# Kernel tuning notes

Hardware: AMD Instinct MI355X
Metric: run time of the kernel (lower is better)

## Reference

```python
import jax, jax.numpy as jnp
import numpy as np

S, P, T, E, H = 32, 48, 8, 64, 64      # scenes, peds/scene, obs_len, embedding_dim, h_dim
D1, D2 = 512, 1024                      # mlp_pre_pool hidden / bottleneck dims
B = S * P
TOTAL_LEN = 20                          # obs_len + pred_len (8 + 12)


def setup_inputs() -> dict:
    key = jax.random.key(0)
    ks = jax.random.split(key, 10)
    h_states = jax.random.normal(ks[0], (1, B, H), jnp.float32)
    end_pos = jax.random.normal(ks[1], (B, 2), jnp.float32)
    traj = jax.random.normal(ks[2], (TOTAL_LEN, B, 2), jnp.float32)
    traj_weight = jax.random.uniform(ks[3], (S, P * P, 2, T), jnp.float32)
    starts = jnp.arange(S, dtype=jnp.int32) * P
    seq_start_end = jnp.stack([starts, starts + P], axis=1)  # uniform scenes of P peds
    # learned params
    W_se = jax.random.normal(ks[4], (T * E, 2 * T), jnp.float32) * 0.05  # spatial_embedding
    b_se = jnp.zeros((T * E,), jnp.float32)
    W1 = jax.random.normal(ks[5], (D1, T * E + H), jnp.float32) * 0.05   # 576 -> 512
    b1 = jnp.zeros((D1,), jnp.float32)
    W2 = jax.random.normal(ks[6], (D2, D1), jnp.float32) * 0.05          # 512 -> 1024
    b2 = jnp.zeros((D2,), jnp.float32)
    return {"h_states": h_states, "seq_start_end": seq_start_end, "end_pos": end_pos,
            "traj": traj, "traj_weight": traj_weight, "mlp_pre_pool_dim_0": T * E,
            "W_se": W_se, "b_se": b_se, "W1": W1, "b1": b1, "W2": W2, "b2": b2}


def reference(h_states, seq_start_end, end_pos, traj, traj_weight, mlp_pre_pool_dim_0,
              W_se, b_se, W1, b1, W2, b2):
    # obs_traj: (obs_len, B, 2) -> (B, T, 2) -> per-scene (S, P, T, 2)
    obs = traj[:T].transpose(1, 0, 2).reshape(S, P, T, 2)
    h = h_states.reshape(S, P, H)
    # pairwise history differences: row (i, j) = obs[j] - obs[i]  (gather-diff)
    rel = obs[:, None, :, :, :] - obs[:, :, None, :, :]          # (S, i, j, T, 2)
    rel = rel.reshape(S, P, P, 2 * T)                            # flatten (T,2) -> 2T
    emb = rel @ W_se.T + b_se                                    # (S, P, P, T*E)
    # traj_weight[i]: (P*P, 2, T) -> permute(0,2,1) -> tile channel to E -> flatten
    w = jnp.transpose(traj_weight, (0, 1, 3, 2))                 # (S, P*P, T, 2)
    w = jnp.tile(w, (1, 1, 1, E // 2)).reshape(S, P, P, T * E)
    emb = w * emb
    # curr_hidden_1: hidden of ped j broadcast over i
    hj = jnp.broadcast_to(h[:, None, :, :], (S, P, P, H))
    x = jnp.concatenate([emb, hj], axis=-1)                      # (S, P, P, 576)
    x = jax.nn.relu(x @ W1.T + b1)                               # (S, P, P, 512)
    x = jax.nn.relu(x @ W2.T + b2)                               # (S, P, P, 1024)
    pool_h = x.max(axis=2)                                       # max over j
    return pool_h.reshape(S * P, D2)
```

## Files before the change

kernel.cpp:

```cpp
#include <hip/hip_runtime.h>
#include <hip/hip_bf16.h>
#include <stdint.h>

#define S_  32
#define P_  48
#define T_  8
#define E_  64
#define H_  64
#define D1_ 512
#define D2_ 1024
#define B_  (S_*P_)
#define M_  (S_*P_*P_)
#define K1_ 576
#define KE_ 512

typedef __attribute__((ext_vector_type(8))) short  short8;
typedef __attribute__((ext_vector_type(8))) __bf16 bf16x8;
typedef __attribute__((ext_vector_type(4))) float  f32x4;
typedef __attribute__((ext_vector_type(8))) float  f32x8;

__device__ inline short f2bf(float x) {
  union { float f; unsigned u; } v; v.f = x;
  unsigned r = v.u + 0x7FFFu + ((v.u >> 16) & 1u);
  return (short)(r >> 16);
}

__device__ inline void async16(const void* g, void* l) {
  __builtin_amdgcn_global_load_lds(
      (const __attribute__((address_space(1))) void*)g,
      (__attribute__((address_space(3))) void*)l, 16, 0, 0);
}

__device__ inline f32x4 mfma16(short8 a, short8 b, f32x4 c) {
  return __builtin_amdgcn_mfma_f32_16x16x32_bf16(
      __builtin_bit_cast(bf16x8, a), __builtin_bit_cast(bf16x8, b), c, 0, 0, 0);
}

__global__ __launch_bounds__(256) void k_cvt_w(const float* __restrict__ W1,
                                               const float* __restrict__ W2,
                                               short* __restrict__ W1b,
                                               short* __restrict__ W2b) {
  int idx = blockIdx.x * 256 + threadIdx.x;
  if (idx < D1_ * K1_) W1b[idx] = f2bf(W1[idx]);
  int idx2 = idx - D1_ * K1_;
  if (idx2 >= 0 && idx2 < D2_ * D1_) W2b[idx2] = f2bf(W2[idx2]);
}

__global__ __launch_bounds__(256) void k_oW(const float* __restrict__ traj,
                                            const float* __restrict__ Wse,
                                            float* __restrict__ oW) {
  int bid = blockIdx.x;
  int p = bid >> 1;
  int n = ((bid & 1) << 8) + threadIdx.x;
  float obs[16];
#pragma unroll
  for (int t = 0; t < T_; ++t) {
    obs[2*t]   = traj[(t*B_ + p)*2 + 0];
    obs[2*t+1] = traj[(t*B_ + p)*2 + 1];
  }
  float acc = 0.f;
#pragma unroll
  for (int k = 0; k < 16; ++k) acc += obs[k] * Wse[n*16 + k];
  oW[p*KE_ + n] = acc;
}

__global__ __launch_bounds__(256) void k_build_x(const float* __restrict__ tw,
                                                 const float* __restrict__ h,
                                                 const float* __restrict__ bse,
                                                 const float* __restrict__ oW,
                                                 short* __restrict__ X) {
  int tid = threadIdx.x;
  int wid = tid >> 6, lane = tid & 63;
  int row = blockIdx.x * 4 + wid;
  int s   = row / (P_ * P_);
  int rem = row - s * (P_ * P_);
  int i   = rem / P_;
  int j   = rem - i * P_;
  int bi = s * P_ + i, bj = s * P_ + j;

  const float* twq = tw + (size_t)(s * (P_*P_) + rem) * 16;
  int t = lane >> 3;
  float w0 = twq[t];
  float w1 = twq[8 + t];

  int n0 = lane * 8;
  f32x8 vj = *(const f32x8*)&oW[(size_t)bj * KE_ + n0];
  f32x8 vi = *(const f32x8*)&oW[(size_t)bi * KE_ + n0];
  f32x8 vb = *(const f32x8*)&bse[n0];
  short8 o;
#pragma unroll
  for (int k = 0; k < 8; ++k) {
    float e = (vj[k] - vi[k] + vb[k]) * ((k & 1) ? w1 : w0);
    o[k] = f2bf(e);
  }
  *(short8*)&X[(size_t)row * K1_ + n0] = o;

  if (lane < 8) {
    f32x8 vh = *(const f32x8*)&h[(size_t)bj * H_ + lane * 8];
    short8 oh;
#pragma unroll
    for (int k = 0; k < 8; ++k) oh[k] = f2bf(vh[k]);
    *(short8*)&X[(size_t)row * K1_ + KE_ + lane * 8] = oh;
  }
}

__global__ __launch_bounds__(512, 2) void k_gemm1(const short* __restrict__ X,
                                                  const short* __restrict__ W1b,
                                                  const float* __restrict__ b1,
                                                  short* __restrict__ X1) {
  __shared__ short Abuf[2][256 * 64];
  __shared__ short Bbuf[2][256 * 64];
  int tid = threadIdx.x;
  int wid = tid >> 6, lane = tid & 63;
  int wgid = (blockIdx.x & 7) * 72 + (blockIdx.x >> 3);
  int tm = wgid >> 1, tn = wgid & 1;
  int brow = tm * 256, bcol = tn * 256;
  int wr = wid >> 2, wc = wid & 3;
  int lr = lane & 15, lhi = lane >> 4;
  int sx = lr & 7;

  f32x4 acc[8][4];
#pragma unroll
  for (int m = 0; m < 8; ++m)
#pragma unroll
    for (int n = 0; n < 4; ++n) acc[m][n] = (f32x4){0.f, 0.f, 0.f, 0.f};

  auto stage = [&](int buf, int k0) {
#pragma unroll
    for (int it = 0; it < 4; ++it) {
      int fg = it * 512 + tid;
      int r = fg >> 3, gs = (fg & 7) ^ (r & 7);
      async16(&X  [(size_t)(brow + r) * K1_ + k0 + (gs << 3)], &Abuf[buf][fg * 8]);
    }
#pragma unroll
    for (int it = 0; it < 4; ++it) {
      int fg = it * 512 + tid;
      int r = fg >> 3, gs = (fg & 7) ^ (r & 7);
      async16(&W1b[(size_t)(bcol + r) * K1_ + k0 + (gs << 3)], &Bbuf[buf][fg * 8]);
    }
  };
  auto compute = [&](int buf) {
#pragma unroll
    for (int kk = 0; kk < 2; ++kk) {
      int gr = kk * 4 + lhi;
      short8 a[8], b[4];
#pragma unroll
      for (int m = 0; m < 8; ++m)
        a[m] = *(const short8*)&Abuf[buf][(wr*128 + m*16 + lr) * 64 + ((gr ^ sx) << 3)];
#pragma unroll
      for (int n = 0; n < 4; ++n)
        b[n] = *(const short8*)&Bbuf[buf][(wc*64 + n*16 + lr) * 64 + ((gr ^ sx) << 3)];
      __builtin_amdgcn_s_setprio(1);
#pragma unroll
      for (int m = 0; m < 8; ++m)
#pragma unroll
        for (int n = 0; n < 4; ++n)
          acc[m][n] = mfma16(a[m], b[n], acc[m][n]);
      __builtin_amdgcn_s_setprio(0);
    }
  };

  stage(0, 0);
  asm volatile("s_waitcnt vmcnt(0)" ::: "memory");
  __builtin_amdgcn_s_barrier();
  for (int t = 0; t < 9; ++t) {
    int cur = t & 1;
    if (t + 1 < 9) stage(cur ^ 1, (t + 1) * 64);
    compute(cur);
    asm volatile("s_waitcnt vmcnt(0)" ::: "memory");
    __builtin_amdgcn_s_barrier();
  }

#pragma unroll
  for (int n = 0; n < 4; ++n) {
    int gcol = bcol + wc*64 + n*16 + lr;
    float bias = b1[gcol];
#pragma unroll
    for (int m = 0; m < 8; ++m) {
      int grow0 = brow + wr*128 + m*16 + lhi*4;
#pragma unroll
      for (int q = 0; q < 4; ++q) {
        float v = acc[m][n][q] + bias;
        v = v > 0.f ? v : 0.f;
        X1[(size_t)(grow0 + q) * D1_ + gcol] = f2bf(v);
      }
    }
  }
}

__global__ __launch_bounds__(512, 2) void k_gemm2(const short* __restrict__ X1,
                                                  const short* __restrict__ W2b,
                                                  const float* __restrict__ b2,
                                                  float* __restrict__ out) {
  __shared__ short Abuf[2][192 * 64];
  __shared__ short Bbuf[2][256 * 64];
  int tid = threadIdx.x;
  int wid = tid >> 6, lane = tid & 63;
  int wgid = (blockIdx.x & 7) * 192 + (blockIdx.x >> 3);
  int tm = wgid >> 2, tn = wgid & 3;
  int brow = tm * 192, bcol = tn * 256;
  int wr = wid >> 2, wc = wid & 3;
  int lr = lane & 15, lhi = lane >> 4;
  int sx = lr & 7;

  f32x4 acc[6][4];
#pragma unroll
  for (int m = 0; m < 6; ++m)
#pragma unroll
    for (int n = 0; n < 4; ++n) acc[m][n] = (f32x4){0.f, 0.f, 0.f, 0.f};

  auto stage = [&](int buf, int k0) {
#pragma unroll
    for (int it = 0; it < 3; ++it) {
      int fg = it * 512 + tid;
      int r = fg >> 3, gs = (fg & 7) ^ (r & 7);
      async16(&X1 [(size_t)(brow + r) * D1_ + k0 + (gs << 3)], &Abuf[buf][fg * 8]);
    }
#pragma unroll
    for (int it = 0; it < 4; ++it) {
      int fg = it * 512 + tid;
      int r = fg >> 3, gs = (fg & 7) ^ (r & 7);
      async16(&W2b[(size_t)(bcol + r) * D1_ + k0 + (gs << 3)], &Bbuf[buf][fg * 8]);
    }
  };
  auto compute = [&](int buf) {
#pragma unroll
    for (int kk = 0; kk < 2; ++kk) {
      int gr = kk * 4 + lhi;
      short8 a[6], b[4];
#pragma unroll
      for (int m = 0; m < 6; ++m)
        a[m] = *(const short8*)&Abuf[buf][(wr*96 + m*16 + lr) * 64 + ((gr ^ sx) << 3)];
#pragma unroll
      for (int n = 0; n < 4; ++n)
        b[n] = *(const short8*)&Bbuf[buf][(wc*64 + n*16 + lr) * 64 + ((gr ^ sx) << 3)];
      __builtin_amdgcn_s_setprio(1);
#pragma unroll
      for (int m = 0; m < 6; ++m)
#pragma unroll
        for (int n = 0; n < 4; ++n)
          acc[m][n] = mfma16(a[m], b[n], acc[m][n]);
      __builtin_amdgcn_s_setprio(0);
    }
  };

  stage(0, 0);
  asm volatile("s_waitcnt vmcnt(0)" ::: "memory");
  __builtin_amdgcn_s_barrier();
  for (int t = 0; t < 8; ++t) {
    int cur = t & 1;
    if (t + 1 < 8) stage(cur ^ 1, (t + 1) * 64);
    compute(cur);
    asm volatile("s_waitcnt vmcnt(0)" ::: "memory");
    __builtin_amdgcn_s_barrier();
  }

  int gbase = tm * 4 + wr * 2;
#pragma unroll
  for (int n = 0; n < 4; ++n) {
    int gcol = bcol + wc*64 + n*16 + lr;
    float bias = b2[gcol];
    float r0 = 0.f, r1 = 0.f;
#pragma unroll
    for (int m = 0; m < 3; ++m)
#pragma unroll
      for (int q = 0; q < 4; ++q) {
        float v0 = acc[m][n][q] + bias;
        float v1 = acc[m + 3][n][q] + bias;
        if (v0 > r0) r0 = v0;
        if (v1 > r1) r1 = v1;
      }
    r0 = fmaxf(r0, __shfl_xor(r0, 16));
    r0 = fmaxf(r0, __shfl_xor(r0, 32));
    r1 = fmaxf(r1, __shfl_xor(r1, 16));
    r1 = fmaxf(r1, __shfl_xor(r1, 32));
    if (lhi == 0) {
      out[(size_t)gbase       * D2_ + gcol] = r0;
      out[(size_t)(gbase + 1) * D2_ + gcol] = r1;
    }
  }
}

extern "C" void kernel_launch(void* const* d_in, const int* in_sizes, int n_in,
                              void* d_out, int out_size, void* d_ws, size_t ws_size,
                              hipStream_t stream) {
  const float* h_states = (const float*)d_in[0];
  const float* traj = (const float*)d_in[3];
  const float* tw   = (const float*)d_in[4];
  const float* Wse  = (const float*)d_in[6];
  const float* bse  = (const float*)d_in[7];
  const float* W1   = (const float*)d_in[8];
  const float* b1   = (const float*)d_in[9];
  const float* W2   = (const float*)d_in[10];
  const float* b2   = (const float*)d_in[11];
  float* out = (float*)d_out;

  char* ws = (char*)d_ws;
  const size_t X_BYTES   = (size_t)M_ * K1_ * 2;
  const size_t X1_BYTES  = (size_t)M_ * D1_ * 2;
  const size_t W1B_BYTES = (size_t)D1_ * K1_ * 2;
  short* X   = (short*)ws;
  short* X1  = (short*)(ws + X_BYTES);
  short* W1b = (short*)(ws + X_BYTES + X1_BYTES);
  short* W2b = (short*)(ws + X_BYTES + X1_BYTES + W1B_BYTES);
  float* oW  = (float*)(ws + X_BYTES);

  k_cvt_w  <<<(D1_*K1_ + D2_*D1_ + 255) / 256, 256, 0, stream>>>(W1, W2, W1b, W2b);
  k_oW     <<<B_ * 2, 256, 0, stream>>>(traj, Wse, oW);
  k_build_x<<<M_ / 4, 256, 0, stream>>>(tw, h_states, bse, oW, X);
  k_gemm1  <<<(M_ / 256) * (D1_ / 256), 512, 0, stream>>>(X, W1b, b1, X1);
  k_gemm2  <<<(M_ / 192) * (D2_ / 256), 512, 0, stream>>>(X1, W2b, b2, out);
}
```

Baseline: 272.2 us.

## Shrink GEMM1 tiles to 128x128 and halve GEMM2 K-step for occupancy

```diff
diff --git a/kernel.cpp b/kernel.cpp
--- a/kernel.cpp
+++ b/kernel.cpp
@@ -104,37 +104,37 @@
   }
 }
 
-__global__ __launch_bounds__(512, 2) void k_gemm1(const short* __restrict__ X,
+__global__ __launch_bounds__(256, 2) void k_gemm1(const short* __restrict__ X,
                                                   const short* __restrict__ W1b,
                                                   const float* __restrict__ b1,
                                                   short* __restrict__ X1) {
-  __shared__ short Abuf[2][256 * 64];
-  __shared__ short Bbuf[2][256 * 64];
+  __shared__ short Abuf[2][128 * 64];
+  __shared__ short Bbuf[2][128 * 64];
   int tid = threadIdx.x;
   int wid = tid >> 6, lane = tid & 63;
-  int wgid = (blockIdx.x & 7) * 72 + (blockIdx.x >> 3);
-  int tm = wgid >> 1, tn = wgid & 1;
-  int brow = tm * 256, bcol = tn * 256;
-  int wr = wid >> 2, wc = wid & 3;
+  int wgid = (blockIdx.x & 7) * 288 + (blockIdx.x >> 3);
+  int tm = wgid >> 2, tn = wgid & 3;
+  int brow = tm * 128, bcol = tn * 128;
+  int wr = wid >> 1, wc = wid & 1;
   int lr = lane & 15, lhi = lane >> 4;
   int sx = lr & 7;
 
-  f32x4 acc[8][4];
-#pragma unroll
-  for (int m = 0; m < 8; ++m)
+  f32x4 acc[4][4];
+#pragma unroll
+  for (int m = 0; m < 4; ++m)
 #pragma unroll
     for (int n = 0; n < 4; ++n) acc[m][n] = (f32x4){0.f, 0.f, 0.f, 0.f};
 
   auto stage = [&](int buf, int k0) {
 #pragma unroll
     for (int it = 0; it < 4; ++it) {
-      int fg = it * 512 + tid;
+      int fg = it * 256 + tid;
       int r = fg >> 3, gs = (fg & 7) ^ (r & 7);
       async16(&X  [(size_t)(brow + r) * K1_ + k0 + (gs << 3)], &Abuf[buf][fg * 8]);
     }
 #pragma unroll
     for (int it = 0; it < 4; ++it) {
-      int fg = it * 512 + tid;
+      int fg = it * 256 + tid;
       int r = fg >> 3, gs = (fg & 7) ^ (r & 7);
       async16(&W1b[(size_t)(bcol + r) * K1_ + k0 + (gs << 3)], &Bbuf[buf][fg * 8]);
     }
@@ -143,16 +143,16 @@
 #pragma unroll
     for (int kk = 0; kk < 2; ++kk) {
       int gr = kk * 4 + lhi;
-      short8 a[8], b[4];
-#pragma unroll
-      for (int m = 0; m < 8; ++m)
-        a[m] = *(const short8*)&Abuf[buf][(wr*128 + m*16 + lr) * 64 + ((gr ^ sx) << 3)];
+      short8 a[4], b[4];
+#pragma unroll
+      for (int m = 0; m < 4; ++m)
+        a[m] = *(const short8*)&Abuf[buf][(wr*64 + m*16 + lr) * 64 + ((gr ^ sx) << 3)];
 #pragma unroll
       for (int n = 0; n < 4; ++n)
         b[n] = *(const short8*)&Bbuf[buf][(wc*64 + n*16 + lr) * 64 + ((gr ^ sx) << 3)];
       __builtin_amdgcn_s_setprio(1);
 #pragma unroll
-      for (int m = 0; m < 8; ++m)
+      for (int m = 0; m < 4; ++m)
 #pragma unroll
         for (int n = 0; n < 4; ++n)
           acc[m][n] = mfma16(a[m], b[n], acc[m][n]);
@@ -176,8 +176,8 @@
     int gcol = bcol + wc*64 + n*16 + lr;
     float bias = b1[gcol];
 #pragma unroll
-    for (int m = 0; m < 8; ++m) {
-      int grow0 = brow + wr*128 + m*16 + lhi*4;
+    for (int m = 0; m < 4; ++m) {
+      int grow0 = brow + wr*64 + m*16 + lhi*4;
 #pragma unroll
       for (int q = 0; q < 4; ++q) {
         float v = acc[m][n][q] + bias;
@@ -188,12 +188,12 @@
   }
 }
 
-__global__ __launch_bounds__(512, 2) void k_gemm2(const short* __restrict__ X1,
+__global__ __launch_bounds__(512, 4) void k_gemm2(const short* __restrict__ X1,
                                                   const short* __restrict__ W2b,
                                                   const float* __restrict__ b2,
                                                   float* __restrict__ out) {
-  __shared__ short Abuf[2][192 * 64];
-  __shared__ short Bbuf[2][256 * 64];
+  __shared__ short Abuf[2][192 * 32];
+  __shared__ short Bbuf[2][256 * 32];
   int tid = threadIdx.x;
   int wid = tid >> 6, lane = tid & 63;
   int wgid = (blockIdx.x & 7) * 192 + (blockIdx.x >> 3);
@@ -201,7 +201,7 @@
   int brow = tm * 192, bcol = tn * 256;
   int wr = wid >> 2, wc = wid & 3;
   int lr = lane & 15, lhi = lane >> 4;
-  int sx = lr & 7;
+  int sx2 = (lr & 3) ^ ((lr >> 2) & 3);
 
   f32x4 acc[6][4];
 #pragma unroll
@@ -209,47 +209,47 @@
 #pragma unroll
     for (int n = 0; n < 4; ++n) acc[m][n] = (f32x4){0.f, 0.f, 0.f, 0.f};
 
+  auto ld1 = [&](int buf, int fg, int k0) {
+    if (fg < 768) {
+      int r = fg >> 2, g = fg & 3;
+      int gs = g ^ (r & 3) ^ ((r >> 2) & 3);
+      async16(&X1 [(size_t)(brow + r) * D1_ + k0 + (gs << 3)], &Abuf[buf][fg * 8]);
+    } else {
+      int fb = fg - 768;
+      int r = fb >> 2, g = fb & 3;
+      int gs = g ^ (r & 3) ^ ((r >> 2) & 3);
+      async16(&W2b[(size_t)(bcol + r) * D1_ + k0 + (gs << 3)], &Bbuf[buf][fb * 8]);
+    }
+  };
   auto stage = [&](int buf, int k0) {
 #pragma unroll
-    for (int it = 0; it < 3; ++it) {
-      int fg = it * 512 + tid;
-      int r = fg >> 3, gs = (fg & 7) ^ (r & 7);
-      async16(&X1 [(size_t)(brow + r) * D1_ + k0 + (gs << 3)], &Abuf[buf][fg * 8]);
-    }
-#pragma unroll
-    for (int it = 0; it < 4; ++it) {
-      int fg = it * 512 + tid;
-      int r = fg >> 3, gs = (fg & 7) ^ (r & 7);
-      async16(&W2b[(size_t)(bcol + r) * D1_ + k0 + (gs << 3)], &Bbuf[buf][fg * 8]);
-    }
+    for (int it = 0; it < 3; ++it) ld1(buf, it * 512 + tid, k0);
+    if (tid < 256) ld1(buf, 1536 + tid, k0);
   };
   auto compute = [&](int buf) {
-#pragma unroll
-    for (int kk = 0; kk < 2; ++kk) {
-      int gr = kk * 4 + lhi;
-      short8 a[6], b[4];
-#pragma unroll
-      for (int m = 0; m < 6; ++m)
-        a[m] = *(const short8*)&Abuf[buf][(wr*96 + m*16 + lr) * 64 + ((gr ^ sx) << 3)];
+    int gr = lhi;
+    short8 a[6], b[4];
+#pragma unroll
+    for (int m = 0; m < 6; ++m)
+      a[m] = *(const short8*)&Abuf[buf][(wr*96 + m*16 + lr) * 32 + ((gr ^ sx2) << 3)];
+#pragma unroll
+    for (int n = 0; n < 4; ++n)
+      b[n] = *(const short8*)&Bbuf[buf][(wc*64 + n*16 + lr) * 32 + ((gr ^ sx2) << 3)];
+    __builtin_amdgcn_s_setprio(1);
+#pragma unroll
+    for (int m = 0; m < 6; ++m)
 #pragma unroll
       for (int n = 0; n < 4; ++n)
-        b[n] = *(const short8*)&Bbuf[buf][(wc*64 + n*16 + lr) * 64 + ((gr ^ sx) << 3)];
-      __builtin_amdgcn_s_setprio(1);
-#pragma unroll
-      for (int m = 0; m < 6; ++m)
-#pragma unroll
-        for (int n = 0; n < 4; ++n)
-          acc[m][n] = mfma16(a[m], b[n], acc[m][n]);
-      __builtin_amdgcn_s_setprio(0);
-    }
+        acc[m][n] = mfma16(a[m], b[n], acc[m][n]);
+    __builtin_amdgcn_s_setprio(0);
   };
 
   stage(0, 0);
   asm volatile("s_waitcnt vmcnt(0)" ::: "memory");
   __builtin_amdgcn_s_barrier();
-  for (int t = 0; t < 8; ++t) {
+  for (int t = 0; t < 16; ++t) {
     int cur = t & 1;
-    if (t + 1 < 8) stage(cur ^ 1, (t + 1) * 64);
+    if (t + 1 < 16) stage(cur ^ 1, (t + 1) * 32);
     compute(cur);
     asm volatile("s_waitcnt vmcnt(0)" ::: "memory");
     __builtin_amdgcn_s_barrier();
@@ -308,6 +308,6 @@
   k_cvt_w  <<<(D1_*K1_ + D2_*D1_ + 255) / 256, 256, 0, stream>>>(W1, W2, W1b, W2b);
   k_oW     <<<B_ * 2, 256, 0, stream>>>(traj, Wse, oW);
   k_build_x<<<M_ / 4, 256, 0, stream>>>(tw, h_states, bse, oW, X);
-  k_gemm1  <<<(M_ / 256) * (D1_ / 256), 512, 0, stream>>>(X, W1b, b1, X1);
+  k_gemm1  <<<(M_ / 128) * (D1_ / 128), 256, 0, stream>>>(X, W1b, b1, X1);
   k_gemm2  <<<(M_ / 192) * (D2_ / 256), 512, 0, stream>>>(X1, W2b, b2, out);
 }
```

Result: slower. 575.6 us (+111.5%).

## Triple-buffer weight tiles with partial waitcnt and halve gemm1 row tile

Applied to the files above, without the earlier changes.

```diff
diff --git a/kernel.cpp b/kernel.cpp
--- a/kernel.cpp
+++ b/kernel.cpp
@@ -108,30 +108,32 @@
                                                   const short* __restrict__ W1b,
                                                   const float* __restrict__ b1,
                                                   short* __restrict__ X1) {
-  __shared__ short Abuf[2][256 * 64];
-  __shared__ short Bbuf[2][256 * 64];
+  __shared__ short Abuf[2][128 * 64];
+  __shared__ short Bbuf[3][256 * 64];
   int tid = threadIdx.x;
   int wid = tid >> 6, lane = tid & 63;
-  int wgid = (blockIdx.x & 7) * 72 + (blockIdx.x >> 3);
+  int wgid = (blockIdx.x & 7) * 144 + (blockIdx.x >> 3);
   int tm = wgid >> 1, tn = wgid & 1;
-  int brow = tm * 256, bcol = tn * 256;
+  int brow = tm * 128, bcol = tn * 256;
   int wr = wid >> 2, wc = wid & 3;
   int lr = lane & 15, lhi = lane >> 4;
   int sx = lr & 7;
 
-  f32x4 acc[8][4];
-#pragma unroll
-  for (int m = 0; m < 8; ++m)
+  f32x4 acc[4][4];
+#pragma unroll
+  for (int m = 0; m < 4; ++m)
 #pragma unroll
     for (int n = 0; n < 4; ++n) acc[m][n] = (f32x4){0.f, 0.f, 0.f, 0.f};
 
-  auto stage = [&](int buf, int k0) {
-#pragma unroll
-    for (int it = 0; it < 4; ++it) {
+  auto stageA = [&](int buf, int k0) {
+#pragma unroll
+    for (int it = 0; it < 2; ++it) {
       int fg = it * 512 + tid;
       int r = fg >> 3, gs = (fg & 7) ^ (r & 7);
-      async16(&X  [(size_t)(brow + r) * K1_ + k0 + (gs << 3)], &Abuf[buf][fg * 8]);
-    }
+      async16(&X[(size_t)(brow + r) * K1_ + k0 + (gs << 3)], &Abuf[buf][fg * 8]);
+    }
+  };
+  auto stageB = [&](int buf, int k0) {
 #pragma unroll
     for (int it = 0; it < 4; ++it) {
       int fg = it * 512 + tid;
@@ -139,20 +141,20 @@
       async16(&W1b[(size_t)(bcol + r) * K1_ + k0 + (gs << 3)], &Bbuf[buf][fg * 8]);
     }
   };
-  auto compute = [&](int buf) {
+  auto compute = [&](int bA, int bB) {
 #pragma unroll
     for (int kk = 0; kk < 2; ++kk) {
       int gr = kk * 4 + lhi;
-      short8 a[8], b[4];
-#pragma unroll
-      for (int m = 0; m < 8; ++m)
-        a[m] = *(const short8*)&Abuf[buf][(wr*128 + m*16 + lr) * 64 + ((gr ^ sx) << 3)];
+      short8 a[4], b[4];
+#pragma unroll
+      for (int m = 0; m < 4; ++m)
+        a[m] = *(const short8*)&Abuf[bA][(wr*64 + m*16 + lr) * 64 + ((gr ^ sx) << 3)];
 #pragma unroll
       for (int n = 0; n < 4; ++n)
-        b[n] = *(const short8*)&Bbuf[buf][(wc*64 + n*16 + lr) * 64 + ((gr ^ sx) << 3)];
+        b[n] = *(const short8*)&Bbuf[bB][(wc*64 + n*16 + lr) * 64 + ((gr ^ sx) << 3)];
       __builtin_amdgcn_s_setprio(1);
 #pragma unroll
-      for (int m = 0; m < 8; ++m)
+      for (int m = 0; m < 4; ++m)
 #pragma unroll
         for (int n = 0; n < 4; ++n)
           acc[m][n] = mfma16(a[m], b[n], acc[m][n]);
@@ -160,15 +162,18 @@
     }
   };
 
-  stage(0, 0);
-  asm volatile("s_waitcnt vmcnt(0)" ::: "memory");
+  const int NT = 9;
+  stageA(0, 0); stageB(0, 0); stageB(1, 64);
+  asm volatile("s_waitcnt vmcnt(4)" ::: "memory");
   __builtin_amdgcn_s_barrier();
-  for (int t = 0; t < 9; ++t) {
-    int cur = t & 1;
-    if (t + 1 < 9) stage(cur ^ 1, (t + 1) * 64);
-    compute(cur);
-    asm volatile("s_waitcnt vmcnt(0)" ::: "memory");
-    __builtin_amdgcn_s_barrier();
+#pragma unroll
+  for (int t = 0; t < NT; ++t) {
+    if (t + 1 < NT) stageA((t + 1) & 1, (t + 1) * 64);
+    if (t + 2 < NT) stageB((t + 2) % 3, (t + 2) * 64);
+    compute(t & 1, t % 3);
+    if (t + 2 < NT)      { asm volatile("s_waitcnt vmcnt(4)" ::: "memory"); }
+    else if (t + 1 < NT) { asm volatile("s_waitcnt vmcnt(0)" ::: "memory"); }
+    if (t + 1 < NT) __builtin_amdgcn_s_barrier();
   }
 
 #pragma unroll
@@ -176,8 +181,8 @@
     int gcol = bcol + wc*64 + n*16 + lr;
     float bias = b1[gcol];
 #pragma unroll
-    for (int m = 0; m < 8; ++m) {
-      int grow0 = brow + wr*128 + m*16 + lhi*4;
+    for (int m = 0; m < 4; ++m) {
+      int grow0 = brow + wr*64 + m*16 + lhi*4;
 #pragma unroll
       for (int q = 0; q < 4; ++q) {
         float v = acc[m][n][q] + bias;
@@ -193,7 +198,7 @@
                                                   const float* __restrict__ b2,
                                                   float* __restrict__ out) {
   __shared__ short Abuf[2][192 * 64];
-  __shared__ short Bbuf[2][256 * 64];
+  __shared__ short Bbuf[3][256 * 64];
   int tid = threadIdx.x;
   int wid = tid >> 6, lane = tid & 63;
   int wgid = (blockIdx.x & 7) * 192 + (blockIdx.x >> 3);
@@ -209,13 +214,15 @@
 #pragma unroll
     for (int n = 0; n < 4; ++n) acc[m][n] = (f32x4){0.f, 0.f, 0.f, 0.f};
 
-  auto stage = [&](int buf, int k0) {
+  auto stageA = [&](int buf, int k0) {
 #pragma unroll
     for (int it = 0; it < 3; ++it) {
       int fg = it * 512 + tid;
       int r = fg >> 3, gs = (fg & 7) ^ (r & 7);
-      async16(&X1 [(size_t)(brow + r) * D1_ + k0 + (gs << 3)], &Abuf[buf][fg * 8]);
-    }
+      async16(&X1[(size_t)(brow + r) * D1_ + k0 + (gs << 3)], &Abuf[buf][fg * 8]);
+    }
+  };
+  auto stageB = [&](int buf, int k0) {
 #pragma unroll
     for (int it = 0; it < 4; ++it) {
       int fg = it * 512 + tid;
@@ -223,17 +230,17 @@
       async16(&W2b[(size_t)(bcol + r) * D1_ + k0 + (gs << 3)], &Bbuf[buf][fg * 8]);
     }
   };
-  auto compute = [&](int buf) {
+  auto compute = [&](int bA, int bB) {
 #pragma unroll
     for (int kk = 0; kk < 2; ++kk) {
       int gr = kk * 4 + lhi;
       short8 a[6], b[4];
 #pragma unroll
       for (int m = 0; m < 6; ++m)
-        a[m] = *(const short8*)&Abuf[buf][(wr*96 + m*16 + lr) * 64 + ((gr ^ sx) << 3)];
+        a[m] = *(const short8*)&Abuf[bA][(wr*96 + m*16 + lr) * 64 + ((gr ^ sx) << 3)];
 #pragma unroll
       for (int n = 0; n < 4; ++n)
-        b[n] = *(const short8*)&Bbuf[buf][(wc*64 + n*16 + lr) * 64 + ((gr ^ sx) << 3)];
+        b[n] = *(const short8*)&Bbuf[bB][(wc*64 + n*16 + lr) * 64 + ((gr ^ sx) << 3)];
       __builtin_amdgcn_s_setprio(1);
 #pragma unroll
       for (int m = 0; m < 6; ++m)
@@ -244,15 +251,18 @@
     }
   };
 
-  stage(0, 0);
-  asm volatile("s_waitcnt vmcnt(0)" ::: "memory");
+  const int NT = 8;
+  stageA(0, 0); stageB(0, 0); stageB(1, 64);
+  asm volatile("s_waitcnt vmcnt(4)" ::: "memory");
   __builtin_amdgcn_s_barrier();
-  for (int t = 0; t < 8; ++t) {
-    int cur = t & 1;
-    if (t + 1 < 8) stage(cur ^ 1, (t + 1) * 64);
-    compute(cur);
-    asm volatile("s_waitcnt vmcnt(0)" ::: "memory");
-    __builtin_amdgcn_s_barrier();
+#pragma unroll
+  for (int t = 0; t < NT; ++t) {
+    if (t + 1 < NT) stageA((t + 1) & 1, (t + 1) * 64);
+    if (t + 2 < NT) stageB((t + 2) % 3, (t + 2) * 64);
+    compute(t & 1, t % 3);
+    if (t + 2 < NT)      { asm volatile("s_waitcnt vmcnt(4)" ::: "memory"); }
+    else if (t + 1 < NT) { asm volatile("s_waitcnt vmcnt(0)" ::: "memory"); }
+    if (t + 1 < NT) __builtin_amdgcn_s_barrier();
   }
 
   int gbase = tm * 4 + wr * 2;
@@ -308,6 +318,6 @@
   k_cvt_w  <<<(D1_*K1_ + D2_*D1_ + 255) / 256, 256, 0, stream>>>(W1, W2, W1b, W2b);
   k_oW     <<<B_ * 2, 256, 0, stream>>>(traj, Wse, oW);
   k_build_x<<<M_ / 4, 256, 0, stream>>>(tw, h_states, bse, oW, X);
-  k_gemm1  <<<(M_ / 256) * (D1_ / 256), 512, 0, stream>>>(X, W1b, b1, X1);
+  k_gemm1  <<<(M_ / 128) * (D1_ / 256), 512, 0, stream>>>(X, W1b, b1, X1);
   k_gemm2  <<<(M_ / 192) * (D2_ / 256), 512, 0, stream>>>(X1, W2b, b2, out);
 }
```

Result: faster. 258.4 us (-5.1%).
